# Kernel tuning notes

Hardware: AMD Instinct MI355X
Metric: run time of the kernel (lower is better)

Reference implementation:

```python
import jax, jax.numpy as jnp
import numpy as np

EMBED_DIM = 1024
NUM_HEADS = 16
HEAD_DIM = EMBED_DIM // NUM_HEADS
SEG_LENS = [2048, 2048, 4096]
DIL_RATES = [1, 2, 4]
SCALE = 1.0 / np.sqrt(HEAD_DIM)


def _hilbert_perm(L):
    """1D permutation ordering indices of a length-L segment along a Hilbert curve
    on the smallest 2^k x 2^k grid with >= L cells (row-major linearization)."""
    n = 1
    while n * n < L:
        n *= 2
    d = np.arange(n * n)
    x = np.zeros_like(d)
    y = np.zeros_like(d)
    t = d.copy()
    s = 1
    while s < n:
        rx = 1 & (t // 2)
        ry = 1 & (t ^ rx)
        swap = ry == 0
        xr = np.where(swap & (rx == 1), s - 1 - x, x)
        yr = np.where(swap & (rx == 1), s - 1 - y, y)
        x = np.where(swap, yr, xr) + s * rx
        y = np.where(swap, xr, yr) + s * ry
        t = t // 4
        s *= 2
    lin = y * n + x          # linear index visited at each Hilbert distance
    perm = lin[lin < L]      # restrict to valid segment positions
    return np.asarray(perm, dtype=np.int64)

# static per-segment Hilbert permutations and their inverses
_PERMS = [_hilbert_perm(L) for L in SEG_LENS]
_INV_PERMS = [np.argsort(p) for p in _PERMS]


def setup_inputs() -> dict:
    key = jax.random.key(0)
    ks = jax.random.split(key, 5)
    B, S, E = 1, 8192, EMBED_DIM
    x = jax.random.normal(ks[0], (B, S, E), dtype=jnp.float32)
    Wqkv = jax.random.normal(ks[1], (3 * E, E), dtype=jnp.float32) * 0.02
    bqkv = jax.random.normal(ks[2], (3 * E,), dtype=jnp.float32) * 0.02
    Wout = jax.random.normal(ks[3], (E, E), dtype=jnp.float32) * 0.02
    bout = jax.random.normal(ks[4], (E,), dtype=jnp.float32) * 0.02
    return {"x": x, "Wqkv": Wqkv, "bqkv": bqkv, "Wout": Wout, "bout": bout}


def _segment_attention(q, k, v, dil_rate, perm, inv_perm):
    # Hilbert reorder of q/k/v within the segment
    if q.shape[2] > 1:
        q = q[:, :, perm]
        k = k[:, :, perm]
        v = v[:, :, perm]
    # dilation: stride-r subsampling of keys/values (in Hilbert order)
    k_d = k[:, :, ::dil_rate]
    v_d = v[:, :, ::dil_rate]
    scores = jnp.einsum('bhqd,bhkd->bhqk', q, k_d) * SCALE
    out = jnp.einsum('bhqk,bhkd->bhqd', jax.nn.softmax(scores, axis=-1), v_d)
    # reverse Hilbert reorder on the output
    if out.shape[2] > 1:
        out = out[:, :, inv_perm]
    return out


def reference(x, Wqkv, bqkv, Wout, bout):
    B, S, E = x.shape
    H, D = NUM_HEADS, HEAD_DIM
    qkv = x @ Wqkv.T + bqkv                                # [B,S,3E]
    qkv = qkv.reshape(B, S, 3, H, D).transpose(2, 0, 3, 1, 4)  # [3,B,H,S,D]
    q, k, v = qkv[0], qkv[1], qkv[2]
    # disjoint contiguous segment slabs covering the sequence
    outs = []
    pos = 0
    for seg_len, dil, perm, inv in zip(SEG_LENS, DIL_RATES, _PERMS, _INV_PERMS):
        sl = slice(pos, pos + seg_len)
        outs.append(_segment_attention(q[:, :, sl], k[:, :, sl], v[:, :, sl], dil, perm, inv))
        pos += seg_len
    out_h = jnp.concatenate(outs, axis=2)                  # [B,H,S,D]
    out = out_h.transpose(0, 2, 1, 3).reshape(B, S, E)
    return out @ Wout.T + bout
```

## Files before the change

### kernel.cpp

```cpp
#include <hip/hip_runtime.h>
#include <math.h>

typedef short short8 __attribute__((ext_vector_type(8)));
typedef float fx4 __attribute__((ext_vector_type(4)));
typedef float fx16 __attribute__((ext_vector_type(16)));
typedef unsigned short ushort;
typedef unsigned int uint;
typedef uint uint2v __attribute__((ext_vector_type(2)));

#define MFMA16(a, b, c) __builtin_amdgcn_mfma_f32_16x16x32_bf16(a, b, c, 0, 0, 0)
#define MFMA32(a, b, c) __builtin_amdgcn_mfma_f32_32x32x16_bf16(a, b, c, 0, 0, 0)

#define QSCALE 0.180336880f
#define MSHIFT 12.0f

#define BAR() do { asm volatile("" ::: "memory"); __builtin_amdgcn_s_barrier(); asm volatile("" ::: "memory"); } while (0)
#define VMCNT(n) asm volatile("s_waitcnt vmcnt(" #n ")" ::: "memory")

__device__ __forceinline__ ushort f2bf(float f) {
    union { float f; uint u; } v; v.f = f;
    uint r = v.u + 0x7fffu + ((v.u >> 16) & 1u);
    return (ushort)(r >> 16);
}

__device__ __forceinline__ float exp2f_fast(float x) {
    float r; asm("v_exp_f32 %0, %1" : "=v"(r) : "v"(x)); return r;
}

__device__ __forceinline__ uint cvt_pk_bf16(float lo, float hi) {
    uint r; asm("v_cvt_pk_bf16_f32 %0, %1, %2" : "=v"(r) : "v"(lo), "v"(hi)); return r;
}

__device__ __forceinline__ short8 mk8(uint a, uint b, uint c, uint d) {
    union { uint u[4]; short8 s; } x; x.u[0] = a; x.u[1] = b; x.u[2] = c; x.u[3] = d; return x.s;
}

__device__ __forceinline__ void gl_lds16(const void* g, void* l) {
    __builtin_amdgcn_global_load_lds(
        (const __attribute__((address_space(1))) void*)g,
        (__attribute__((address_space(3))) void*)l, 16, 0, 0);
}

__device__ ushort g_XB[8192 * 1024];
__device__ ushort g_WQB[3072 * 1024];
__device__ ushort g_WOB[1024 * 1024];
__device__ ushort g_QSEG[16 * 8192 * 64];
__device__ ushort g_KSEG[16 * 4096 * 64];
__device__ ushort g_VSEG[16 * 4096 * 64];
__device__ ushort g_VT[16 * 64 * 4096];
__device__ ushort g_ATTN[8192 * 1024];
__device__ int g_QROW[8192];
__device__ int g_KVROW[8192];
__device__ int g_KVSRC[4096];

__global__ __launch_bounds__(256) void cvt_kernel(const float* __restrict__ x,
                                                  const float* __restrict__ wq,
                                                  const float* __restrict__ wo) {
    int idx = blockIdx.x * 256 + threadIdx.x;
    const int NX = 8192 * 1024 / 4, NQ = 3072 * 1024 / 4, NO = 1024 * 1024 / 4;
    const float* s; ushort* d; int rel;
    if (idx < NX)            { s = x;  d = g_XB;  rel = idx; }
    else if (idx < NX + NQ)  { s = wq; d = g_WQB; rel = idx - NX; }
    else if (idx < NX + NQ + NO) { s = wo; d = g_WOB; rel = idx - NX - NQ; }
    else return;
    fx4 v = *(const fx4*)(s + (long)rel * 4);
    uint lo = f2bf(v[0]) | ((uint)f2bf(v[1]) << 16);
    uint hi = f2bf(v[2]) | ((uint)f2bf(v[3]) << 16);
    uint2v w; w[0] = lo; w[1] = hi;
    *(uint2v*)(d + (long)rel * 4) = w;
}

__global__ __launch_bounds__(1024) void perm_kernel() {
    __shared__ int perm_lds[4096];
    __shared__ int inv_lds[4096];
    __shared__ int sc[1024];
    int seg = blockIdx.x;
    int L     = (seg == 2) ? 4096 : 2048;
    int dil   = (seg == 0) ? 1 : (seg == 1) ? 2 : 4;
    int pos   = (seg == 0) ? 0 : (seg == 1) ? 2048 : 4096;
    int kbase = (seg == 0) ? 0 : (seg == 1) ? 2048 : 3072;
    int tid = threadIdx.x;

    int lin[4]; int flg[4]; int cnt = 0;
    #pragma unroll
    for (int c = 0; c < 4; c++) {
        int d = tid * 4 + c;
        int x = 0, y = 0, t = d;
        for (int s = 1; s < 64; s <<= 1) {
            int rx = (t >> 1) & 1;
            int ry = (t ^ rx) & 1;
            if (ry == 0) {
                if (rx == 1) { x = s - 1 - x; y = s - 1 - y; }
                int tmp = x; x = y; y = tmp;
            }
            x += s * rx; y += s * ry; t >>= 2;
        }
        lin[c] = y * 64 + x;
        flg[c] = (lin[c] < L) ? 1 : 0;
        cnt += flg[c];
    }
    sc[tid] = cnt; __syncthreads();
    for (int off = 1; off < 1024; off <<= 1) {
        int v = sc[tid];
        int a = (tid >= off) ? sc[tid - off] : 0;
        __syncthreads();
        sc[tid] = v + a;
        __syncthreads();
    }
    int base = sc[tid] - cnt;
    #pragma unroll
    for (int c = 0; c < 4; c++) if (flg[c]) perm_lds[base++] = lin[c];
    __syncthreads();
    for (int i = tid; i < L; i += 1024) inv_lds[perm_lds[i]] = i;
    __syncthreads();
    for (int p = tid; p < L; p += 1024) {
        int i = inv_lds[p];
        int s = pos + p;
        g_QROW[s] = pos + i;
        if ((i & (dil - 1)) == 0) {
            int kr = kbase + i / dil;
            g_KVROW[s] = kr;
            g_KVSRC[kr] = s;
        } else {
            g_KVROW[s] = -1;
        }
    }
}


#define GEMM_DEFS                                                             \
    const int tid = threadIdx.x;                                              \
    const int lane = tid & 63;                                                \
    const int wid = tid >> 6;                                                 \
    const int lq = lane & 15, lg = lane >> 4;                                 \
    const int swz = lq & 7;                                                   \
    const int wr = wid >> 2, wc = wid & 3;

#define LD_A(cur)                                                             \
    _Pragma("unroll")                                                         \
    for (int mi = 0; mi < 4; mi++)                                            \
        _Pragma("unroll")                                                     \
        for (int kk = 0; kk < 2; kk++)                                        \
            af[mi][kk] = *(const short8*)(&AT[cur][(wr * 64 + mi * 16 + lq) * 64 + (((kk * 4 + lg) ^ swz) << 3)]);
#define LD_B0(cur)                                                            \
    _Pragma("unroll")                                                         \
    for (int nj = 0; nj < 2; nj++)                                            \
        _Pragma("unroll")                                                     \
        for (int kk = 0; kk < 2; kk++)                                        \
            bf0[nj][kk] = *(const short8*)(&BT[cur][(wc * 32 + nj * 16 + lq) * 64 + (((kk * 4 + lg) ^ swz) << 3)]);
#define LD_B1(cur)                                                            \
    _Pragma("unroll")                                                         \
    for (int nj = 0; nj < 2; nj++)                                            \
        _Pragma("unroll")                                                     \
        for (int kk = 0; kk < 2; kk++)                                        \
            bf1[nj][kk] = *(const short8*)(&BT[cur][(128 + wc * 32 + nj * 16 + lq) * 64 + (((kk * 4 + lg) ^ swz) << 3)]);
#define MM0()                                                                 \
    __builtin_amdgcn_s_setprio(1);                                            \
    _Pragma("unroll")                                                         \
    for (int kk = 0; kk < 2; kk++)                                            \
        _Pragma("unroll")                                                     \
        for (int mi = 0; mi < 4; mi++)                                        \
            _Pragma("unroll")                                                 \
            for (int nj = 0; nj < 2; nj++)                                    \
                acc[mi][nj] = MFMA16(af[mi][kk], bf0[nj][kk], acc[mi][nj]);    \
    __builtin_amdgcn_s_setprio(0);
#define MM1()                                                                 \
    __builtin_amdgcn_s_setprio(1);                                            \
    _Pragma("unroll")                                                         \
    for (int kk = 0; kk < 2; kk++)                                            \
        _Pragma("unroll")                                                     \
        for (int mi = 0; mi < 4; mi++)                                        \
            _Pragma("unroll")                                                 \
            for (int nj = 0; nj < 2; nj++)                                    \
                acc[mi][nj + 2] = MFMA16(af[mi][kk], bf1[nj][kk], acc[mi][nj + 2]); \
    __builtin_amdgcn_s_setprio(0);

#define STG_A(b, kt_) do { gl_lds16(sA0 + (kt_) * 64, &AT[b][ca0 * 8]);      \
                           gl_lds16(sA1 + (kt_) * 64, &AT[b][ca1 * 8]); } while (0)
#define STG_B0(b, kt_) do { gl_lds16(sB[0] + (kt_) * 64, &BT[b][tid * 8]);   \
                            gl_lds16(sB[1] + (kt_) * 64, &BT[b][(tid + 512) * 8]); } while (0)
#define STG_B1(b, kt_) do { gl_lds16(sB[2] + (kt_) * 64, &BT[b][(tid + 1024) * 8]); \
                            gl_lds16(sB[3] + (kt_) * 64, &BT[b][(tid + 1536) * 8]); } while (0)

#define GEMM_MAIN_LOOP                                                        \
    STG_A(0, 0); STG_B0(0, 0); STG_B1(0, 0);                                  \
    VMCNT(2);                                                                 \
    BAR();                                                                    \
    for (int kt = 0; kt < 15; kt++) {                                         \
        int cur = kt & 1, nxt = cur ^ 1;                                      \
        LD_A(cur); LD_B0(cur);                                                \
        STG_A(nxt, kt + 1); STG_B0(nxt, kt + 1);                              \
        MM0();                                                                \
        VMCNT(4);                                                             \
        BAR();                                                                \
        LD_B1(cur);                                                           \
        STG_B1(nxt, kt + 1);                                                  \
        MM1();                                                                \
        VMCNT(2);                                                             \
        BAR();                                                                \
    }                                                                         \
    LD_A(1); LD_B0(1);                                                        \
    MM0();                                                                    \
    VMCNT(0);                                                                 \
    BAR();                                                                    \
    LD_B1(1);                                                                 \
    MM1();

__global__ __launch_bounds__(512, 2) void qkv_merged(const float* __restrict__ bias) {
    __shared__ __align__(16) ushort AT[2][128 * 64];
    __shared__ __align__(16) ushort BT[2][256 * 64];
    GEMM_DEFS
    int b = blockIdx.x;
    bool isQ = b < 256;
    int bx, by;
    if (isQ) { bx = b & 63; by = b >> 6; }
    else     { int t = b - 256; bx = t & 31; by = t >> 5; }
    const int row0 = bx * 128, col0 = by * 256;

    int ca0 = tid, ca1 = tid + 512;
    int ra0 = ca0 >> 3, pa0 = (ca0 & 7) ^ (ra0 & 7);
    int ra1 = ca1 >> 3, pa1 = (ca1 & 7) ^ (ra1 & 7);
    long arow0 = isQ ? (row0 + ra0) : g_KVSRC[row0 + ra0];
    long arow1 = isQ ? (row0 + ra1) : g_KVSRC[row0 + ra1];
    const ushort* sA0 = g_XB + arow0 * 1024 + pa0 * 8;
    const ushort* sA1 = g_XB + arow1 * 1024 + pa1 * 8;
    int bcol0 = isQ ? col0 : (1024 + col0);
    const ushort* sB[4];
    #pragma unroll
    for (int j = 0; j < 4; j++) {
        int c = tid + 512 * j;
        int r = c >> 3, p = (c & 7) ^ (r & 7);
        sB[j] = g_WQB + (long)(bcol0 + r) * 1024 + p * 8;
    }

    fx4 acc[4][4] = {};
    short8 af[4][2], bf0[2][2], bf1[2][2];

    GEMM_MAIN_LOOP

    if (isQ) {
        #pragma unroll
        for (int mi = 0; mi < 4; mi++)
            #pragma unroll
            for (int r = 0; r < 4; r++) {
                int m = row0 + wr * 64 + mi * 16 + lg * 4 + r;
                int qr = g_QROW[m];
                #pragma unroll
                for (int nj = 0; nj < 4; nj++) {
                    int n = col0 + (nj >> 1) * 128 + wc * 32 + (nj & 1) * 16 + lq;
                    float val = acc[mi][nj][r] + bias[n];
                    int h = n >> 6, dd = n & 63;
                    g_QSEG[((long)h * 8192 + qr) * 64 + dd] = f2bf(val * QSCALE);
                }
            }
    } else {
        #pragma unroll
        for (int mi = 0; mi < 4; mi++)
            #pragma unroll
            for (int r = 0; r < 4; r++) {
                int m = row0 + wr * 64 + mi * 16 + lg * 4 + r;
                #pragma unroll
                for (int nj = 0; nj < 4; nj++) {
                    int n = col0 + (nj >> 1) * 128 + wc * 32 + (nj & 1) * 16 + lq;
                    float val = acc[mi][nj][r] + bias[1024 + n];
                    int h = (n >> 6) & 15, dd = n & 63;
                    if (n < 1024) g_KSEG[((long)h * 4096 + m) * 64 + dd] = f2bf(val);
                    else          g_VSEG[((long)h * 4096 + m) * 64 + dd] = f2bf(val);
                }
            }
    }
}

__global__ __launch_bounds__(512, 2) void out_gemm8(const float* __restrict__ bias,
                                                    float* __restrict__ out) {
    __shared__ __align__(16) ushort AT[2][128 * 64];
    __shared__ __align__(16) ushort BT[2][256 * 64];
    GEMM_DEFS
    const int row0 = blockIdx.x * 128, col0 = blockIdx.y * 256;

    int ca0 = tid, ca1 = tid + 512;
    int ra0 = ca0 >> 3, pa0 = (ca0 & 7) ^ (ra0 & 7);
    int ra1 = ca1 >> 3, pa1 = (ca1 & 7) ^ (ra1 & 7);
    const ushort* sA0 = g_ATTN + (long)g_QROW[row0 + ra0] * 1024 + pa0 * 8;
    const ushort* sA1 = g_ATTN + (long)g_QROW[row0 + ra1] * 1024 + pa1 * 8;
    const ushort* sB[4];
    #pragma unroll
    for (int j = 0; j < 4; j++) {
        int c = tid + 512 * j;
        int r = c >> 3, p = (c & 7) ^ (r & 7);
        sB[j] = g_WOB + (long)(col0 + r) * 1024 + p * 8;
    }

    fx4 acc[4][4] = {};
    short8 af[4][2], bf0[2][2], bf1[2][2];

    GEMM_MAIN_LOOP

    #pragma unroll
    for (int mi = 0; mi < 4; mi++)
        #pragma unroll
        for (int r = 0; r < 4; r++) {
            int mm = row0 + wr * 64 + mi * 16 + lg * 4 + r;
            #pragma unroll
            for (int nj = 0; nj < 4; nj++) {
                int n = col0 + (nj >> 1) * 128 + wc * 32 + (nj & 1) * 16 + lq;
                out[(long)mm * 1024 + n] = acc[mi][nj][r] + bias[n];
            }
        }
}

__global__ __launch_bounds__(256) void vtrans_kernel() {
    __shared__ __align__(16) ushort tile[64 * 80];
    int b = blockIdx.x; int h = b >> 6; int rt = b & 63;
    const ushort* src = g_VSEG + ((long)h * 4096 + rt * 64) * 64;
    int tid = threadIdx.x;
    for (int c = tid; c < 512; c += 256) {
        int row = c >> 3, ch = c & 7;
        *(short8*)&tile[row * 80 + ch * 8] = *(const short8*)(src + row * 64 + ch * 8);
    }
    __syncthreads();
    for (int c = tid; c < 512; c += 256) {
        int d = c >> 3, oc = c & 7;
        ushort tmp[8];
        #pragma unroll
        for (int e = 0; e < 8; e++) tmp[e] = tile[(oc * 8 + e) * 80 + d];
        *(short8*)&g_VT[((long)h * 64 + d) * 4096 + rt * 64 + oc * 8] = *(short8*)tmp;
    }
}

__global__ __launch_bounds__(256, 4) void attn_kernel() {
    __shared__ __align__(16) ushort Kt[2][64 * 64];
    __shared__ __align__(16) ushort Vt[2][64 * 64];
    int bid = blockIdx.x;
    int seg, h, qblk;
    if (bid < 256)      { seg = 0; h = bid >> 4;         qblk = bid & 15; }
    else if (bid < 512) { seg = 1; h = (bid - 256) >> 4; qblk = (bid - 256) & 15; }
    else                { seg = 2; h = (bid - 512) >> 5; qblk = (bid - 512) & 31; }
    int qbase = (seg == 0) ? 0 : (seg == 1) ? 2048 : 4096;
    int kbase = (seg == 0) ? 0 : (seg == 1) ? 2048 : 3072;
    int nkt   = (seg == 0) ? 32 : 16;

    int tid = threadIdx.x;
    int lane = tid & 63, wid = tid >> 6;
    int l5 = lane & 31, hi = lane >> 5;
    int sw7 = l5 & 7;
    int qrow0 = qbase + qblk * 128 + wid * 32;

    const ushort* kseg = g_KSEG + (long)h * 4096 * 64;
    const ushort* vtb0 = g_VT + (long)h * 64 * 4096 + kbase;

    int c0 = tid, c1 = tid + 256;
    int r0 = c0 >> 3, e0 = (c0 & 7) ^ (r0 & 7);
    int r1 = c1 >> 3, e1 = (c1 & 7) ^ (r1 & 7);
    const ushort* ka0 = kseg + (long)(kbase + r0) * 64 + e0 * 8;
    const ushort* ka1 = kseg + (long)(kbase + r1) * 64 + e1 * 8;
    const ushort* va0 = vtb0 + (long)r0 * 4096 + e0 * 8;
    const ushort* va1 = vtb0 + (long)r1 * 4096 + e1 * 8;

#define STAGE(b, kt_) do {                                                    \
        gl_lds16(ka0 + (long)(kt_) * 4096, &Kt[b][c0 * 8]);                   \
        gl_lds16(ka1 + (long)(kt_) * 4096, &Kt[b][c1 * 8]);                   \
        gl_lds16(va0 + (kt_) * 64, &Vt[b][c0 * 8]);                           \
        gl_lds16(va1 + (kt_) * 64, &Vt[b][c1 * 8]);                           \
    } while (0)

    const ushort* qp = g_QSEG + ((long)h * 8192 + qrow0 + l5) * 64;
    short8 qf[4];
    #pragma unroll
    for (int dc = 0; dc < 4; dc++)
        qf[dc] = *(const short8*)(qp + dc * 16 + hi * 8);

    short8 onesA;
    #pragma unroll
    for (int i = 0; i < 8; i++) onesA[i] = (short)0x3F80;

    STAGE(0, 0);
    VMCNT(0);
    __syncthreads();

    fx16 accO0 = {}, accO1 = {};
    fx16 lacc = {};

    for (int kt = 0; kt < nkt; kt++) {
        int cur = kt & 1;
        if (kt + 1 < nkt) STAGE(cur ^ 1, kt + 1);
        const ushort* Kc = Kt[cur];
        const ushort* Vc = Vt[cur];

        fx16 s0 = {}, s1 = {};
        __builtin_amdgcn_s_setprio(1);
        #pragma unroll
        for (int dc = 0; dc < 4; dc++) {
            short8 kf0 = *(const short8*)(Kc + l5 * 64 + (((2 * dc + hi) ^ sw7) << 3));
            short8 kf1 = *(const short8*)(Kc + (32 + l5) * 64 + (((2 * dc + hi) ^ sw7) << 3));
            s0 = MFMA32(kf0, qf[dc], s0);
            s1 = MFMA32(kf1, qf[dc], s1);
        }
        __builtin_amdgcn_s_setprio(0);

        uint dw0[8], dw1[8];
        #pragma unroll
        for (int i = 0; i < 8; i++) {
            float p0 = exp2f_fast(s0[2 * i] - MSHIFT);
            float p1 = exp2f_fast(s0[2 * i + 1] - MSHIFT);
            float p2 = exp2f_fast(s1[2 * i] - MSHIFT);
            float p3 = exp2f_fast(s1[2 * i + 1] - MSHIFT);
            dw0[i] = cvt_pk_bf16(p0, p1);
            dw1[i] = cvt_pk_bf16(p2, p3);
        }

        short8 pb[4];
        #pragma unroll
        for (int m4 = 0; m4 < 4; m4++) {
            int i0 = (m4 & 1) * 4;
            uint a0 = (m4 >> 1) ? dw1[i0] : dw0[i0];
            uint a1 = (m4 >> 1) ? dw1[i0 + 1] : dw0[i0 + 1];
            uint b0 = (m4 >> 1) ? dw1[i0 + 2] : dw0[i0 + 2];
            uint b1 = (m4 >> 1) ? dw1[i0 + 3] : dw0[i0 + 3];
            uint2v ra = __builtin_amdgcn_permlane32_swap(a0, b0, false, false);
            uint2v rb = __builtin_amdgcn_permlane32_swap(a1, b1, false, false);
            pb[m4] = mk8(ra[0], rb[0], ra[1], rb[1]);
        }

        __builtin_amdgcn_s_setprio(1);
        #pragma unroll
        for (int m4 = 0; m4 < 4; m4++) {
            short8 vf0 = *(const short8*)(Vc + l5 * 64 + (((2 * m4 + hi) ^ sw7) << 3));
            short8 vf1 = *(const short8*)(Vc + (32 + l5) * 64 + (((2 * m4 + hi) ^ sw7) << 3));
            lacc = MFMA32(onesA, pb[m4], lacc);
            accO0 = MFMA32(vf0, pb[m4], accO0);
            accO1 = MFMA32(vf1, pb[m4], accO1);
        }
        __builtin_amdgcn_s_setprio(0);

        VMCNT(0);
        __syncthreads();
    }
#undef STAGE

    float ri = 1.0f / lacc[0];
    ushort* op = g_ATTN + (long)(qrow0 + l5) * 1024 + h * 64;
    #pragma unroll
    for (int i = 0; i < 8; i++) {
        uint w0 = cvt_pk_bf16(accO0[2 * i] * ri, accO0[2 * i + 1] * ri);
        uint w1 = cvt_pk_bf16(accO1[2 * i] * ri, accO1[2 * i + 1] * ri);
        int d0 = 2 * (i & 1) + 8 * (i >> 1) + 4 * hi;
        *(uint*)(op + d0) = w0;
        *(uint*)(op + 32 + d0) = w1;
    }
}

extern "C" void kernel_launch(void* const* d_in, const int* in_sizes, int n_in,
                              void* d_out, int out_size, void* d_ws, size_t ws_size,
                              hipStream_t stream) {
    const float* x    = (const float*)d_in[0];
    const float* Wqkv = (const float*)d_in[1];
    const float* bqkv = (const float*)d_in[2];
    const float* Wout = (const float*)d_in[3];
    const float* bout = (const float*)d_in[4];
    float* out = (float*)d_out;
    (void)d_ws; (void)ws_size; (void)in_sizes; (void)n_in; (void)out_size;

    cvt_kernel<<<dim3(12288), dim3(256), 0, stream>>>(x, Wqkv, Wout);
    perm_kernel<<<dim3(3), dim3(1024), 0, stream>>>();
    qkv_merged<<<dim3(512), dim3(512), 0, stream>>>(bqkv);
    vtrans_kernel<<<dim3(1024), dim3(256), 0, stream>>>();
    attn_kernel<<<dim3(1024), dim3(256), 0, stream>>>();
    out_gemm8<<<dim3(64, 4), dim3(512), 0, stream>>>(bout, out);
}
```

Baseline: 155.4 us.

## Merge convert and permutation kernels, unroll attention loop by two, drop exp shift

Fuses the fp32-to-bf16 conversion kernel and the Hilbert permutation kernel into a single launch with 1024-thread blocks, removing one kernel launch. The attention key-tile loop is unrolled by two so the double-buffer index becomes a compile-time constant, which may simplify LDS addressing. The constant max-shift subtraction before exp2 is dropped, saving one op per score but relying on scores staying small enough not to overflow in bf16/fp32. The unrolled loop assumes an even tile count, and the large shared-memory arrays are now reserved by conversion blocks too, which may lower their occupancy.

```diff
diff --git a/kernel.cpp b/kernel.cpp
--- a/kernel.cpp
+++ b/kernel.cpp
@@ -12,7 +12,6 @@
 #define MFMA32(a, b, c) __builtin_amdgcn_mfma_f32_32x32x16_bf16(a, b, c, 0, 0, 0)
 
 #define QSCALE 0.180336880f
-#define MSHIFT 12.0f
 
 #define BAR() do { asm volatile("" ::: "memory"); __builtin_amdgcn_s_barrier(); asm volatile("" ::: "memory"); } while (0)
 #define VMCNT(n) asm volatile("s_waitcnt vmcnt(" #n ")" ::: "memory")
@@ -53,49 +52,49 @@
 __device__ int g_KVROW[8192];
 __device__ int g_KVSRC[4096];
 
-__global__ __launch_bounds__(256) void cvt_kernel(const float* __restrict__ x,
-                                                  const float* __restrict__ wq,
-                                                  const float* __restrict__ wo) {
-    int idx = blockIdx.x * 256 + threadIdx.x;
-    const int NX = 8192 * 1024 / 4, NQ = 3072 * 1024 / 4, NO = 1024 * 1024 / 4;
-    const float* s; ushort* d; int rel;
-    if (idx < NX)            { s = x;  d = g_XB;  rel = idx; }
-    else if (idx < NX + NQ)  { s = wq; d = g_WQB; rel = idx - NX; }
-    else if (idx < NX + NQ + NO) { s = wo; d = g_WOB; rel = idx - NX - NQ; }
-    else return;
-    fx4 v = *(const fx4*)(s + (long)rel * 4);
-    uint lo = f2bf(v[0]) | ((uint)f2bf(v[1]) << 16);
-    uint hi = f2bf(v[2]) | ((uint)f2bf(v[3]) << 16);
-    uint2v w; w[0] = lo; w[1] = hi;
-    *(uint2v*)(d + (long)rel * 4) = w;
-}
-
-__global__ __launch_bounds__(1024) void perm_kernel() {
+__global__ __launch_bounds__(1024) void cvtperm_kernel(const float* __restrict__ x,
+                                                       const float* __restrict__ wq,
+                                                       const float* __restrict__ wo) {
     __shared__ int perm_lds[4096];
     __shared__ int inv_lds[4096];
     __shared__ int sc[1024];
-    int seg = blockIdx.x;
+    int b = blockIdx.x;
+    int tid = threadIdx.x;
+    if (b >= 3) {
+        int idx = (b - 3) * 1024 + tid;
+        const int NX = 8192 * 1024 / 4, NQ = 3072 * 1024 / 4;
+        const float* s; ushort* d; int rel;
+        if (idx < NX)           { s = x;  d = g_XB;  rel = idx; }
+        else if (idx < NX + NQ) { s = wq; d = g_WQB; rel = idx - NX; }
+        else                    { s = wo; d = g_WOB; rel = idx - NX - NQ; }
+        fx4 v = *(const fx4*)(s + (long)rel * 4);
+        uint lo = f2bf(v[0]) | ((uint)f2bf(v[1]) << 16);
+        uint hi = f2bf(v[2]) | ((uint)f2bf(v[3]) << 16);
+        uint2v w; w[0] = lo; w[1] = hi;
+        *(uint2v*)(d + (long)rel * 4) = w;
+        return;
+    }
+    int seg = b;
     int L     = (seg == 2) ? 4096 : 2048;
     int dil   = (seg == 0) ? 1 : (seg == 1) ? 2 : 4;
     int pos   = (seg == 0) ? 0 : (seg == 1) ? 2048 : 4096;
     int kbase = (seg == 0) ? 0 : (seg == 1) ? 2048 : 3072;
-    int tid = threadIdx.x;
 
     int lin[4]; int flg[4]; int cnt = 0;
     #pragma unroll
     for (int c = 0; c < 4; c++) {
         int d = tid * 4 + c;
-        int x = 0, y = 0, t = d;
+        int px = 0, py = 0, t = d;
         for (int s = 1; s < 64; s <<= 1) {
             int rx = (t >> 1) & 1;
             int ry = (t ^ rx) & 1;
             if (ry == 0) {
-                if (rx == 1) { x = s - 1 - x; y = s - 1 - y; }
-                int tmp = x; x = y; y = tmp;
+                if (rx == 1) { px = s - 1 - px; py = s - 1 - py; }
+                int tmp = px; px = py; py = tmp;
             }
-            x += s * rx; y += s * ry; t >>= 2;
+            px += s * rx; py += s * ry; t >>= 2;
         }
-        lin[c] = y * 64 + x;
+        lin[c] = py * 64 + px;
         flg[c] = (lin[c] < L) ? 1 : 0;
         cnt += flg[c];
     }
@@ -381,61 +380,61 @@
     fx16 accO0 = {}, accO1 = {};
     fx16 lacc = {};
 
-    for (int kt = 0; kt < nkt; kt++) {
-        int cur = kt & 1;
-        if (kt + 1 < nkt) STAGE(cur ^ 1, kt + 1);
-        const ushort* Kc = Kt[cur];
-        const ushort* Vc = Vt[cur];
-
-        fx16 s0 = {}, s1 = {};
-        __builtin_amdgcn_s_setprio(1);
-        #pragma unroll
-        for (int dc = 0; dc < 4; dc++) {
-            short8 kf0 = *(const short8*)(Kc + l5 * 64 + (((2 * dc + hi) ^ sw7) << 3));
-            short8 kf1 = *(const short8*)(Kc + (32 + l5) * 64 + (((2 * dc + hi) ^ sw7) << 3));
-            s0 = MFMA32(kf0, qf[dc], s0);
-            s1 = MFMA32(kf1, qf[dc], s1);
-        }
-        __builtin_amdgcn_s_setprio(0);
-
-        uint dw0[8], dw1[8];
-        #pragma unroll
-        for (int i = 0; i < 8; i++) {
-            float p0 = exp2f_fast(s0[2 * i] - MSHIFT);
-            float p1 = exp2f_fast(s0[2 * i + 1] - MSHIFT);
-            float p2 = exp2f_fast(s1[2 * i] - MSHIFT);
-            float p3 = exp2f_fast(s1[2 * i + 1] - MSHIFT);
-            dw0[i] = cvt_pk_bf16(p0, p1);
-            dw1[i] = cvt_pk_bf16(p2, p3);
-        }
-
-        short8 pb[4];
-        #pragma unroll
-        for (int m4 = 0; m4 < 4; m4++) {
-            int i0 = (m4 & 1) * 4;
-            uint a0 = (m4 >> 1) ? dw1[i0] : dw0[i0];
-            uint a1 = (m4 >> 1) ? dw1[i0 + 1] : dw0[i0 + 1];
-            uint b0 = (m4 >> 1) ? dw1[i0 + 2] : dw0[i0 + 2];
-            uint b1 = (m4 >> 1) ? dw1[i0 + 3] : dw0[i0 + 3];
-            uint2v ra = __builtin_amdgcn_permlane32_swap(a0, b0, false, false);
-            uint2v rb = __builtin_amdgcn_permlane32_swap(a1, b1, false, false);
-            pb[m4] = mk8(ra[0], rb[0], ra[1], rb[1]);
-        }
-
-        __builtin_amdgcn_s_setprio(1);
-        #pragma unroll
-        for (int m4 = 0; m4 < 4; m4++) {
-            short8 vf0 = *(const short8*)(Vc + l5 * 64 + (((2 * m4 + hi) ^ sw7) << 3));
-            short8 vf1 = *(const short8*)(Vc + (32 + l5) * 64 + (((2 * m4 + hi) ^ sw7) << 3));
-            lacc = MFMA32(onesA, pb[m4], lacc);
-            accO0 = MFMA32(vf0, pb[m4], accO0);
-            accO1 = MFMA32(vf1, pb[m4], accO1);
-        }
-        __builtin_amdgcn_s_setprio(0);
-
-        VMCNT(0);
-        __syncthreads();
-    }
+#define AITER(cur, kt_) do {                                                  \
+        if ((kt_) + 1 < nkt) STAGE((cur) ^ 1, (kt_) + 1);                     \
+        const ushort* Kc = Kt[cur];                                           \
+        const ushort* Vc = Vt[cur];                                           \
+        fx16 s0 = {}, s1 = {};                                                \
+        __builtin_amdgcn_s_setprio(1);                                        \
+        _Pragma("unroll")                                                     \
+        for (int dc = 0; dc < 4; dc++) {                                      \
+            short8 kf0 = *(const short8*)(Kc + l5 * 64 + (((2 * dc + hi) ^ sw7) << 3)); \
+            short8 kf1 = *(const short8*)(Kc + (32 + l5) * 64 + (((2 * dc + hi) ^ sw7) << 3)); \
+            s0 = MFMA32(kf0, qf[dc], s0);                                     \
+            s1 = MFMA32(kf1, qf[dc], s1);                                     \
+        }                                                                     \
+        __builtin_amdgcn_s_setprio(0);                                        \
+        uint dw0[8], dw1[8];                                                  \
+        _Pragma("unroll")                                                     \
+        for (int i = 0; i < 8; i++) {                                         \
+            float p0 = exp2f_fast(s0[2 * i]);                                 \
+            float p1 = exp2f_fast(s0[2 * i + 1]);                             \
+            float p2 = exp2f_fast(s1[2 * i]);                                 \
+            float p3 = exp2f_fast(s1[2 * i + 1]);                             \
+            dw0[i] = cvt_pk_bf16(p0, p1);                                     \
+            dw1[i] = cvt_pk_bf16(p2, p3);                                     \
+        }                                                                     \
+        short8 pb[4];                                                         \
+        _Pragma("unroll")                                                     \
+        for (int m4 = 0; m4 < 4; m4++) {                                      \
+            int i0 = (m4 & 1) * 4;                                            \
+            uint a0 = (m4 >> 1) ? dw1[i0] : dw0[i0];                          \
+            uint a1 = (m4 >> 1) ? dw1[i0 + 1] : dw0[i0 + 1];                  \
+            uint b0 = (m4 >> 1) ? dw1[i0 + 2] : dw0[i0 + 2];                  \
+            uint b1 = (m4 >> 1) ? dw1[i0 + 3] : dw0[i0 + 3];                  \
+            uint2v ra = __builtin_amdgcn_permlane32_swap(a0, b0, false, false); \
+            uint2v rb = __builtin_amdgcn_permlane32_swap(a1, b1, false, false); \
+            pb[m4] = mk8(ra[0], rb[0], ra[1], rb[1]);                         \
+        }                                                                     \
+        __builtin_amdgcn_s_setprio(1);                                        \
+        _Pragma("unroll")                                                     \
+        for (int m4 = 0; m4 < 4; m4++) {                                      \
+            short8 vf0 = *(const short8*)(Vc + l5 * 64 + (((2 * m4 + hi) ^ sw7) << 3)); \
+            short8 vf1 = *(const short8*)(Vc + (32 + l5) * 64 + (((2 * m4 + hi) ^ sw7) << 3)); \
+            lacc = MFMA32(onesA, pb[m4], lacc);                               \
+            accO0 = MFMA32(vf0, pb[m4], accO0);                               \
+            accO1 = MFMA32(vf1, pb[m4], accO1);                               \
+        }                                                                     \
+        __builtin_amdgcn_s_setprio(0);                                        \
+        VMCNT(0);                                                             \
+        __syncthreads();                                                      \
+    } while (0)
+
+    for (int kt = 0; kt < nkt; kt += 2) {
+        AITER(0, kt);
+        AITER(1, kt + 1);
+    }
+#undef AITER
 #undef STAGE
 
     float ri = 1.0f / lacc[0];
@@ -461,8 +460,7 @@
     float* out = (float*)d_out;
     (void)d_ws; (void)ws_size; (void)in_sizes; (void)n_in; (void)out_size;
 
-    cvt_kernel<<<dim3(12288), dim3(256), 0, stream>>>(x, Wqkv, Wout);
-    perm_kernel<<<dim3(3), dim3(1024), 0, stream>>>();
+    cvtperm_kernel<<<dim3(3075), dim3(1024), 0, stream>>>(x, Wqkv, Wout);
     qkv_merged<<<dim3(512), dim3(512), 0, stream>>>(bqkv);
     vtrans_kernel<<<dim3(1024), dim3(256), 0, stream>>>();
     attn_kernel<<<dim3(1024), dim3(256), 0, stream>>>();
```

New measurement: 149.6 us (median of 3 runs). 3.7% less time.
